# Optimization experiments

Hardware: AMD Instinct MI355X
Metric: run time of the kernel (lower is better)

## Reference

```python
import jax, jax.numpy as jnp
import numpy as np

N = 100000   # nodes
E = 800000   # edges
D = 128      # input dim
H = 128      # hidden dim
C = 2        # output classes
BN_EPS = 1e-5


def setup_inputs() -> dict:
    key = jax.random.key(0)
    ks = jax.random.split(key, 24)
    glorot = lambda k, shape: jax.random.normal(k, shape, dtype=jnp.float32) * np.sqrt(2.0 / (shape[0] + shape[1]))
    inp = {
        "x": jax.random.normal(ks[0], (N, D), dtype=jnp.float32),
        "edge_index": jax.random.randint(ks[1], (2, E), 0, N, dtype=jnp.int64),
        "W0": glorot(ks[2], (D, H)), "b0": jnp.zeros((H,), jnp.float32),
        "W1": glorot(ks[3], (H, H)), "b1": jnp.zeros((H,), jnp.float32),
        "W2": glorot(ks[4], (H, H)), "b2": jnp.zeros((H,), jnp.float32),
        "W3": glorot(ks[5], (H, C)), "b3": jnp.zeros((C,), jnp.float32),
        # BatchNorm (eval mode: running stats)
        "bn0_g": jax.random.normal(ks[6], (H,), dtype=jnp.float32) * 0.1 + 1.0,
        "bn0_b": jax.random.normal(ks[7], (H,), dtype=jnp.float32) * 0.1,
        "bn0_m": jax.random.normal(ks[8], (H,), dtype=jnp.float32) * 0.1,
        "bn0_v": jax.random.uniform(ks[9], (H,), dtype=jnp.float32) + 0.5,
        "bn1_g": jax.random.normal(ks[10], (H,), dtype=jnp.float32) * 0.1 + 1.0,
        "bn1_b": jax.random.normal(ks[11], (H,), dtype=jnp.float32) * 0.1,
        "bn1_m": jax.random.normal(ks[12], (H,), dtype=jnp.float32) * 0.1,
        "bn1_v": jax.random.uniform(ks[13], (H,), dtype=jnp.float32) + 0.5,
    }
    return inp


def _gcn_conv(h, W, b, src, dst, norm, self_norm):
    # GCNConv: D^-1/2 (A + I) D^-1/2 (h W) + b
    hw = h @ W                                             # [N, out]
    msg = hw[src] * norm[:, None]                          # [E, out] gather
    agg = jax.ops.segment_sum(msg, dst, num_segments=N)    # [N, out] scatter-add
    return agg + hw * self_norm[:, None] + b


def _bn_eval(h, g, b, m, v):
    return (h - m) * (g * jax.lax.rsqrt(v + BN_EPS)) + b


def reference(x, edge_index, W0, b0, W1, b1, W2, b2, W3, b3,
              bn0_g, bn0_b, bn0_m, bn0_v, bn1_g, bn1_b, bn1_m, bn1_v):
    src, dst = edge_index[0], edge_index[1]
    # symmetric normalization with self-loops
    deg = jax.ops.segment_sum(jnp.ones((E,), jnp.float32), dst, num_segments=N) + 1.0
    dis = jax.lax.rsqrt(deg)                 # deg >= 1, no inf
    norm = dis[src] * dis[dst]               # per-edge norm
    self_norm = dis * dis                    # self-loop norm

    # layer 0 (eval mode: dropout is identity)
    h = jax.nn.relu(_gcn_conv(x, W0, b0, src, dst, norm, self_norm))
    # layer 1: conv -> bn -> relu -> residual
    h_prev = h
    h = _gcn_conv(h, W1, b1, src, dst, norm, self_norm)
    h = jax.nn.relu(_bn_eval(h, bn0_g, bn0_b, bn0_m, bn0_v)) + h_prev
    # layer 2
    h_prev = h
    h = _gcn_conv(h, W2, b2, src, dst, norm, self_norm)
    h = jax.nn.relu(_bn_eval(h, bn1_g, bn1_b, bn1_m, bn1_v)) + h_prev
    # output layer
    h = _gcn_conv(h, W3, b3, src, dst, norm, self_norm)
    return jax.nn.log_softmax(h, axis=1)
```

## Files before the change

### kernel.cpp

```cpp
#include <hip/hip_runtime.h>
#include <hip/hip_bf16.h>
#include <type_traits>

#define NN 100000
#define NE 800000
#define HD 128
#define BN_EPS 1e-5f
#define NB_E_C 3125

typedef __bf16 bf16x8 __attribute__((ext_vector_type(8)));
typedef float  f32x4  __attribute__((ext_vector_type(4)));
typedef float  f32x2  __attribute__((ext_vector_type(2)));


__global__ __launch_bounds__(256) void count_prep_k(const int* __restrict__ ei, int* __restrict__ count,
                                                    int* __restrict__ rank,
                                                    const float* __restrict__ W0, const float* __restrict__ W1,
                                                    const float* __restrict__ W2, __bf16* __restrict__ WT,
                                                    const float* __restrict__ g0, const float* __restrict__ b0,
                                                    const float* __restrict__ m0, const float* __restrict__ v0,
                                                    const float* __restrict__ g1, const float* __restrict__ b1,
                                                    const float* __restrict__ m1, const float* __restrict__ v1,
                                                    float* __restrict__ A0, float* __restrict__ B0,
                                                    float* __restrict__ A1, float* __restrict__ B1) {
    int bid = blockIdx.x;
    int tid = threadIdx.x;
    if (bid < NB_E_C) {
        int e = bid * 256 + tid;
        if (e < NE) rank[e] = atomicAdd(&count[ei[NE + e]], 1);
    } else if (bid < NB_E_C + 3) {
        int w = bid - NB_E_C;
        const float* Ws[3] = {W0, W1, W2};
        const float* W = Ws[w];
        __bf16* T = WT + w * (HD * HD);
        #pragma unroll 4
        for (int it = 0; it < 64; ++it) {
            int idx = it * 256 + tid;
            int n = idx >> 7, k = idx & 127;
            T[idx] = (__bf16)W[k * HD + n];
        }
    } else {
        if (tid < 128) {
            float a = g0[tid] * rsqrtf(v0[tid] + BN_EPS);
            A0[tid] = a; B0[tid] = b0[tid] - m0[tid] * a;
        } else {
            int u = tid - 128;
            float a = g1[u] * rsqrtf(v1[u] + BN_EPS);
            A1[u] = a; B1[u] = b1[u] - m1[u] * a;
        }
    }
}

__global__ __launch_bounds__(256) void scan1_k(const int* __restrict__ count,
                                               int* __restrict__ rp, int* __restrict__ bsums,
                                               float* __restrict__ dis, float* __restrict__ selfn) {
    __shared__ int sm[256];
    int tid = threadIdx.x;
    int i = blockIdx.x * 256 + tid;
    int v = (i < NN) ? count[i] : 0;
    if (i < NN) {
        float deg = (float)v + 1.0f;
        float di = rsqrtf(deg);
        dis[i] = di;
        selfn[i] = di * di;
    }
    sm[tid] = v; __syncthreads();
    for (int off = 1; off < 256; off <<= 1) {
        int t = (tid >= off) ? sm[tid - off] : 0;
        __syncthreads();
        sm[tid] += t;
        __syncthreads();
    }
    if (i < NN) rp[i] = sm[tid] - v;
    if (tid == 255) bsums[blockIdx.x] = sm[tid];
}

__global__ __launch_bounds__(256) void scan23_k(int* __restrict__ rp, const int* __restrict__ bsums, int nb) {
    __shared__ int sm[256];
    int tid = threadIdx.x;
    int b = blockIdx.x;
    int partial = 0;
    for (int i = tid; i < b; i += 256) partial += bsums[i];
    sm[tid] = partial; __syncthreads();
    #pragma unroll
    for (int off = 128; off > 0; off >>= 1) {
        if (tid < off) sm[tid] += sm[tid + off];
        __syncthreads();
    }
    int prefix = sm[0];
    int i = b * 256 + tid;
    if (i < NN) rp[i] += prefix;
    if (i == 0) rp[NN] = NE;
}

__global__ __launch_bounds__(256) void scatter_k(const int* __restrict__ ei, const int* __restrict__ rp,
                                                 const int* __restrict__ rank, const float* __restrict__ dis,
                                                 uint2* __restrict__ edges) {
    int e = blockIdx.x * 256 + threadIdx.x;
    if (e >= NE) return;
    int s = ei[e], d = ei[NE + e];
    int pos = rp[d] + rank[e];
    edges[pos] = make_uint2((unsigned)s, __float_as_uint(dis[s] * dis[d]));
}


template <typename T>
__global__ __launch_bounds__(256, 5) void gemm128_k(const T* __restrict__ A, const __bf16* __restrict__ WTg,
                                                    __bf16* __restrict__ HW) {
    __shared__ __bf16 WL[128 * 128];
    const int tid = threadIdx.x;
    const int wid  = __builtin_amdgcn_readfirstlane(tid >> 6);
    const int lane = tid & 63;
    const int m = lane & 15, quad = lane >> 4;
    const int row_base = blockIdx.x * 64 + wid * 16;

    int r = row_base + m;
    if (r >= NN) r = NN - 1;
    bf16x8 afr[4];
    if constexpr (std::is_same<T, float>::value) {
        const float4* ap = (const float4*)(A + (size_t)r * HD);
        #pragma unroll
        for (int ks = 0; ks < 4; ++ks) {
            float4 x0 = ap[ks * 8 + quad * 2], x1 = ap[ks * 8 + quad * 2 + 1];
            bf16x8 a;
            a[0] = (__bf16)x0.x; a[1] = (__bf16)x0.y; a[2] = (__bf16)x0.z; a[3] = (__bf16)x0.w;
            a[4] = (__bf16)x1.x; a[5] = (__bf16)x1.y; a[6] = (__bf16)x1.z; a[7] = (__bf16)x1.w;
            afr[ks] = a;
        }
    } else {
        const bf16x8* ap = (const bf16x8*)(A + (size_t)r * HD);
        #pragma unroll
        for (int ks = 0; ks < 4; ++ks) afr[ks] = ap[ks * 4 + quad];
    }

    #pragma unroll
    for (int it = 0; it < 8; ++it) {
        int id = it * 256 + tid;
        int n = id >> 4, c = id & 15;
        int cs = c ^ ((n >> 3) & 7);
        *(uint4*)&WL[n * 128 + cs * 8] = *(const uint4*)(WTg + n * HD + c * 8);
    }
    __syncthreads();

    f32x4 acc[8];
    #pragma unroll
    for (int ct = 0; ct < 8; ++ct) acc[ct] = (f32x4){0.f, 0.f, 0.f, 0.f};

    #pragma unroll
    for (int ks = 0; ks < 4; ++ks) {
        #pragma unroll
        for (int ct = 0; ct < 8; ++ct) {
            int n = m * 8 + ct;
            int cs = (ks * 4 + quad) ^ (m & 7);
            bf16x8 bfr = *(const bf16x8*)&WL[n * 128 + cs * 8];
            acc[ct] = __builtin_amdgcn_mfma_f32_16x16x32_bf16(afr[ks], bfr, acc[ct], 0, 0, 0);
        }
    }

    #pragma unroll
    for (int rr = 0; rr < 4; ++rr) {
        int row = row_base + quad * 4 + rr;
        if (row < NN) {
            bf16x8 v;
            #pragma unroll
            for (int ct = 0; ct < 8; ++ct) v[ct] = (__bf16)acc[ct][rr];
            *(bf16x8*)(HW + (size_t)row * HD + m * 8) = v;
        }
    }
}


__device__ __forceinline__ void acc8p(f32x2* acc, uint4 rv, float wt) {
    f32x2 w2 = {wt, wt};
    f32x2 x0 = {__uint_as_float(rv.x << 16), __uint_as_float(rv.x & 0xffff0000u)};
    f32x2 x1 = {__uint_as_float(rv.y << 16), __uint_as_float(rv.y & 0xffff0000u)};
    f32x2 x2 = {__uint_as_float(rv.z << 16), __uint_as_float(rv.z & 0xffff0000u)};
    f32x2 x3 = {__uint_as_float(rv.w << 16), __uint_as_float(rv.w & 0xffff0000u)};
    acc[0] = __builtin_elementwise_fma(x0, w2, acc[0]);
    acc[1] = __builtin_elementwise_fma(x1, w2, acc[1]);
    acc[2] = __builtin_elementwise_fma(x2, w2, acc[2]);
    acc[3] = __builtin_elementwise_fma(x3, w2, acc[3]);
}

__device__ __forceinline__ void unpack8(uint4 rv, float* f) {
    f[0] = __uint_as_float(rv.x << 16);         f[1] = __uint_as_float(rv.x & 0xffff0000u);
    f[2] = __uint_as_float(rv.y << 16);         f[3] = __uint_as_float(rv.y & 0xffff0000u);
    f[4] = __uint_as_float(rv.z << 16);         f[5] = __uint_as_float(rv.z & 0xffff0000u);
    f[6] = __uint_as_float(rv.w << 16);         f[7] = __uint_as_float(rv.w & 0xffff0000u);
}

template <int MODE>
__global__ __launch_bounds__(256) void agg_k(const __bf16* __restrict__ hw, const int* __restrict__ rp,
                                             const uint2* __restrict__ edges,
                                             const float* __restrict__ selfn, const float* __restrict__ bias,
                                             const float* __restrict__ bnA, const float* __restrict__ bnB,
                                             __bf16* __restrict__ hb, const float* __restrict__ W3,
                                             float2* __restrict__ hw3) {
    const int lane = threadIdx.x & 63;
    const int wid  = threadIdx.x >> 6;
    const int grp  = lane >> 4;
    const int m    = lane & 15;
    const int n = blockIdx.x * 16 + wid * 4 + grp;
    const int c0 = m * 8;
    const int L = NE - 1;

    const int e0 = rp[n], e1 = rp[n + 1];

    const float sn = selfn[n];
    uint4 rv_self = *(const uint4*)(hw + ((size_t)n << 7) + c0);
    __bf16* hbp = hb + ((size_t)n << 7) + c0;
    uint4 rv_prev;
    float4 bs0 = *(const float4*)(bias + c0);
    float4 bs1 = *(const float4*)(bias + c0 + 4);
    float4 a0v, a1v, b0v, b1v;
    float4 w0, w1, w2, w3v;
    if (MODE != 0) {
        rv_prev = *(const uint4*)hbp;
        a0v = *(const float4*)(bnA + c0); a1v = *(const float4*)(bnA + c0 + 4);
        b0v = *(const float4*)(bnB + c0); b1v = *(const float4*)(bnB + c0 + 4);
    }
    if (MODE == 2) {
        w0  = *(const float4*)(W3 + c0 * 2);
        w1  = *(const float4*)(W3 + c0 * 2 + 4);
        w2  = *(const float4*)(W3 + c0 * 2 + 8);
        w3v = *(const float4*)(W3 + c0 * 2 + 12);
    }

    f32x2 acc2[4];
    #pragma unroll
    for (int j = 0; j < 4; ++j) acc2[j] = (f32x2){0.f, 0.f};

    int e = e0;
    int cnt = e1 - e0;
    uint2 edA = edges[min(e,     L)];
    uint2 edB = edges[min(e + 1, L)];
    uint2 edC = edges[min(e + 2, L)];
    uint2 edD = edges[min(e + 3, L)];
    while (cnt >= 4) {
        uint4 r0 = *(const uint4*)(hw + ((size_t)edA.x << 7) + c0);
        uint4 r1 = *(const uint4*)(hw + ((size_t)edB.x << 7) + c0);
        uint4 r2 = *(const uint4*)(hw + ((size_t)edC.x << 7) + c0);
        uint4 r3 = *(const uint4*)(hw + ((size_t)edD.x << 7) + c0);
        uint2 nA = edges[min(e + 4, L)];
        uint2 nB = edges[min(e + 5, L)];
        uint2 nC = edges[min(e + 6, L)];
        uint2 nD = edges[min(e + 7, L)];
        acc8p(acc2, r0, __uint_as_float(edA.y));
        acc8p(acc2, r1, __uint_as_float(edB.y));
        acc8p(acc2, r2, __uint_as_float(edC.y));
        acc8p(acc2, r3, __uint_as_float(edD.y));
        edA = nA; edB = nB; edC = nC; edD = nD;
        e += 4; cnt -= 4;
    }
    if (cnt >= 2) {
        uint4 r0 = *(const uint4*)(hw + ((size_t)edA.x << 7) + c0);
        uint4 r1 = *(const uint4*)(hw + ((size_t)edB.x << 7) + c0);
        acc8p(acc2, r0, __uint_as_float(edA.y));
        acc8p(acc2, r1, __uint_as_float(edB.y));
        edA = edC;
        cnt -= 2;
    }
    if (cnt == 1) {
        uint4 rv = *(const uint4*)(hw + ((size_t)edA.x << 7) + c0);
        acc8p(acc2, rv, __uint_as_float(edA.y));
    }
    acc8p(acc2, rv_self, sn);

    float acc[8] = {acc2[0][0], acc2[0][1], acc2[1][0], acc2[1][1],
                    acc2[2][0], acc2[2][1], acc2[3][0], acc2[3][1]};

    float z[8] = {acc[0] + bs0.x, acc[1] + bs0.y, acc[2] + bs0.z, acc[3] + bs0.w,
                  acc[4] + bs1.x, acc[5] + bs1.y, acc[6] + bs1.z, acc[7] + bs1.w};

    if (MODE == 0) {
        bf16x8 v;
        #pragma unroll
        for (int j = 0; j < 8; ++j) v[j] = (__bf16)fmaxf(z[j], 0.f);
        *(bf16x8*)hbp = v;
    } else {
        float Af[8] = {a0v.x, a0v.y, a0v.z, a0v.w, a1v.x, a1v.y, a1v.z, a1v.w};
        float Bf[8] = {b0v.x, b0v.y, b0v.z, b0v.w, b1v.x, b1v.y, b1v.z, b1v.w};
        float pr[8];
        unpack8(rv_prev, pr);
        float hn[8];
        #pragma unroll
        for (int j = 0; j < 8; ++j)
            hn[j] = fmaxf(fmaf(z[j], Af[j], Bf[j]), 0.f) + pr[j];

        if (MODE == 1) {
            bf16x8 v;
            #pragma unroll
            for (int j = 0; j < 8; ++j) v[j] = (__bf16)hn[j];
            *(bf16x8*)hbp = v;
        } else {
            float p0 = hn[0] * w0.x + hn[1] * w0.z + hn[2] * w1.x + hn[3] * w1.z
                     + hn[4] * w2.x + hn[5] * w2.z + hn[6] * w3v.x + hn[7] * w3v.z;
            float p1 = hn[0] * w0.y + hn[1] * w0.w + hn[2] * w1.y + hn[3] * w1.w
                     + hn[4] * w2.y + hn[5] * w2.w + hn[6] * w3v.y + hn[7] * w3v.w;
            #pragma unroll
            for (int o = 1; o < 16; o <<= 1) {
                p0 += __shfl_xor(p0, o);
                p1 += __shfl_xor(p1, o);
            }
            if (m == 0) hw3[n] = make_float2(p0, p1);
        }
    }
}


__global__ __launch_bounds__(256) void final_k(const float2* __restrict__ hw3, const int* __restrict__ rp,
                                               const uint2* __restrict__ edges,
                                               const float* __restrict__ selfn, const float* __restrict__ b3,
                                               float* __restrict__ out) {
    int n = blockIdx.x * 256 + threadIdx.x;
    if (n >= NN) return;
    const int L = NE - 1;
    float a0 = 0.f, a1 = 0.f;
    int e0 = rp[n], e1 = rp[n + 1];
    int cnt = e1 - e0;
    uint2 edA = edges[min(e0,     L)];
    uint2 edB = edges[min(e0 + 1, L)];
    int e = e0;
    while (cnt >= 2) {
        float2 v0 = hw3[edA.x];
        float2 v1 = hw3[edB.x];
        float w0 = __uint_as_float(edA.y), w1 = __uint_as_float(edB.y);
        edA = edges[min(e + 2, L)];
        edB = edges[min(e + 3, L)];
        a0 = fmaf(w0, v0.x, a0); a1 = fmaf(w0, v0.y, a1);
        a0 = fmaf(w1, v1.x, a0); a1 = fmaf(w1, v1.y, a1);
        e += 2; cnt -= 2;
    }
    if (cnt == 1) {
        float2 v = hw3[edA.x];
        float w = __uint_as_float(edA.y);
        a0 = fmaf(w, v.x, a0); a1 = fmaf(w, v.y, a1);
    }
    float sn = selfn[n];
    float2 hv = hw3[n];
    float z0 = a0 + sn * hv.x + b3[0];
    float z1 = a1 + sn * hv.y + b3[1];
    float mx = fmaxf(z0, z1);
    float l = mx + logf(expf(z0 - mx) + expf(z1 - mx));
    out[n * 2 + 0] = z0 - l;
    out[n * 2 + 1] = z1 - l;
}


extern "C" void kernel_launch(void* const* d_in, const int* in_sizes, int n_in,
                              void* d_out, int out_size, void* d_ws, size_t ws_size,
                              hipStream_t stream) {
    (void)in_sizes; (void)n_in; (void)out_size; (void)ws_size;

    const float* x   = (const float*)d_in[0];
    const int*   ei  = (const int*)d_in[1];
    const float* W0  = (const float*)d_in[2];
    const float* b0  = (const float*)d_in[3];
    const float* W1  = (const float*)d_in[4];
    const float* b1  = (const float*)d_in[5];
    const float* W2  = (const float*)d_in[6];
    const float* b2  = (const float*)d_in[7];
    const float* W3  = (const float*)d_in[8];
    const float* b3  = (const float*)d_in[9];
    const float* bn0g = (const float*)d_in[10];
    const float* bn0b = (const float*)d_in[11];
    const float* bn0m = (const float*)d_in[12];
    const float* bn0v = (const float*)d_in[13];
    const float* bn1g = (const float*)d_in[14];
    const float* bn1b = (const float*)d_in[15];
    const float* bn1m = (const float*)d_in[16];
    const float* bn1v = (const float*)d_in[17];
    float* out = (float*)d_out;

    char* p = (char*)d_ws;
    auto alloc = [&](size_t bytes) -> void* {
        void* r = (void*)p;
        p += (bytes + 255) & ~(size_t)255;
        return r;
    };
    __bf16*  hb    = (__bf16*)alloc((size_t)NN * HD * 2);
    __bf16*  hw    = (__bf16*)alloc((size_t)NN * HD * 2);
    float2*  hw3   = (float2*)alloc((size_t)NN * 8);
    float*   dis   = (float*)alloc((size_t)NN * 4);
    float*   selfn = (float*)alloc((size_t)NN * 4);
    int*     count = (int*)alloc((size_t)NN * 4);
    int*     rp    = (int*)alloc((size_t)(NN + 1) * 4);
    uint2*   edges = (uint2*)alloc((size_t)NE * 8);
    int*     rank  = (int*)alloc((size_t)NE * 4);
    int*     bsums = (int*)alloc((size_t)512 * 4);
    float*   bnA0  = (float*)alloc(128 * 4);
    float*   bnB0  = (float*)alloc(128 * 4);
    float*   bnA1  = (float*)alloc(128 * 4);
    float*   bnB1  = (float*)alloc(128 * 4);
    __bf16*  WT    = (__bf16*)alloc((size_t)3 * HD * HD * 2);

    const int NB_E = (NE + 255) / 256;
    const int NB_N = (NN + 255) / 256;
    const int NB_G = (NN + 63) / 64;
    const int NB_A = (NN + 15) / 16;

    hipMemsetAsync(count, 0, (size_t)NN * 4, stream);

    count_prep_k<<<NB_E + 4, 256, 0, stream>>>(ei, count, rank,
                                               W0, W1, W2, WT,
                                               bn0g, bn0b, bn0m, bn0v, bn1g, bn1b, bn1m, bn1v,
                                               bnA0, bnB0, bnA1, bnB1);
    scan1_k<<<NB_N, 256, 0, stream>>>(count, rp, bsums, dis, selfn);
    scan23_k<<<NB_N, 256, 0, stream>>>(rp, bsums, NB_N);
    scatter_k<<<NB_E, 256, 0, stream>>>(ei, rp, rank, dis, edges);

    gemm128_k<float><<<NB_G, 256, 0, stream>>>(x, WT, hw);
    agg_k<0><<<NB_A, 256, 0, stream>>>(hw, rp, edges, selfn, b0,
                                       nullptr, nullptr, hb, nullptr, nullptr);
    gemm128_k<__bf16><<<NB_G, 256, 0, stream>>>(hb, WT + HD * HD, hw);
    agg_k<1><<<NB_A, 256, 0, stream>>>(hw, rp, edges, selfn, b1,
                                       bnA0, bnB0, hb, nullptr, nullptr);
    gemm128_k<__bf16><<<NB_G, 256, 0, stream>>>(hb, WT + 2 * HD * HD, hw);
    agg_k<2><<<NB_A, 256, 0, stream>>>(hw, rp, edges, selfn, b2,
                                       bnA1, bnB1, hb, W3, hw3);
    final_k<<<NB_N, 256, 0, stream>>>(hw3, rp, edges, selfn, b3, out);
}
```

Measured before the change: 334.5 us.

## Sort edges by source block within rows and order nodes by degree

The CSR build now counts edges per (destination, source-block) pair across 16 source blocks. Each row's edges therefore come out grouped by source range, which should improve gather locality in the aggregation kernels. It also builds a degree histogram and a permutation that orders nodes by in-degree, so each aggregation wavefront handles rows of similar length and lane imbalance drops. The costs are a 16x larger count array to memset and scan, an extra indirection through perm in every agg kernel, and scattered output writes; some parameter loads are also moved later in agg_k to shorten register live ranges.

```diff
diff --git a/kernel.cpp b/kernel.cpp
--- a/kernel.cpp
+++ b/kernel.cpp
@@ -7,14 +7,17 @@
 #define HD 128
 #define BN_EPS 1e-5f
 #define NB_E_C 3125
+#define NB_N_C 391
+#define NKB 16
+#define KBW 6250
 
 typedef __bf16 bf16x8 __attribute__((ext_vector_type(8)));
 typedef float  f32x4  __attribute__((ext_vector_type(4)));
 typedef float  f32x2  __attribute__((ext_vector_type(2)));
 
 
-__global__ __launch_bounds__(256) void count_prep_k(const int* __restrict__ ei, int* __restrict__ count,
-                                                    int* __restrict__ rank,
+__global__ __launch_bounds__(256) void count_prep_k(const int* __restrict__ ei, int* __restrict__ count2,
+                                                    int* __restrict__ rank2,
                                                     const float* __restrict__ W0, const float* __restrict__ W1,
                                                     const float* __restrict__ W2, __bf16* __restrict__ WT,
                                                     const float* __restrict__ g0, const float* __restrict__ b0,
@@ -27,7 +30,11 @@
     int tid = threadIdx.x;
     if (bid < NB_E_C) {
         int e = bid * 256 + tid;
-        if (e < NE) rank[e] = atomicAdd(&count[ei[NE + e]], 1);
+        if (e < NE) {
+            int s = ei[e], d = ei[NE + e];
+            int kb = s / KBW;
+            rank2[e] = atomicAdd(&count2[d * NKB + kb], 1);
+        }
     } else if (bid < NB_E_C + 3) {
         int w = bid - NB_E_C;
         const float* Ws[3] = {W0, W1, W2};
@@ -51,19 +58,39 @@
     }
 }
 
-__global__ __launch_bounds__(256) void scan1_k(const int* __restrict__ count,
+__global__ __launch_bounds__(256) void scan1_k(int* __restrict__ count2,
                                                int* __restrict__ rp, int* __restrict__ bsums,
-                                               float* __restrict__ dis, float* __restrict__ selfn) {
+                                               float* __restrict__ dis, float* __restrict__ selfn,
+                                               int* __restrict__ hist) {
     __shared__ int sm[256];
+    __shared__ int lhist[64];
     int tid = threadIdx.x;
+    if (tid < 64) lhist[tid] = 0;
     int i = blockIdx.x * 256 + tid;
-    int v = (i < NN) ? count[i] : 0;
+    int v = 0;
     if (i < NN) {
+        int base = i * NKB;
+        int4* c4 = (int4*)&count2[base];
+        int4 a = c4[0], b = c4[1], c = c4[2], d = c4[3];
+        int run = 0;
+        int t;
+        t = a.x; a.x = run; run += t;  t = a.y; a.y = run; run += t;
+        t = a.z; a.z = run; run += t;  t = a.w; a.w = run; run += t;
+        t = b.x; b.x = run; run += t;  t = b.y; b.y = run; run += t;
+        t = b.z; b.z = run; run += t;  t = b.w; b.w = run; run += t;
+        t = c.x; c.x = run; run += t;  t = c.y; c.y = run; run += t;
+        t = c.z; c.z = run; run += t;  t = c.w; c.w = run; run += t;
+        t = d.x; d.x = run; run += t;  t = d.y; d.y = run; run += t;
+        t = d.z; d.z = run; run += t;  t = d.w; d.w = run; run += t;
+        c4[0] = a; c4[1] = b; c4[2] = c; c4[3] = d;
+        v = run;
         float deg = (float)v + 1.0f;
         float di = rsqrtf(deg);
         dis[i] = di;
         selfn[i] = di * di;
     }
+    __syncthreads();
+    if (i < NN) atomicAdd(&lhist[min(v, 63)], 1);
     sm[tid] = v; __syncthreads();
     for (int off = 1; off < 256; off <<= 1) {
         int t = (tid >= off) ? sm[tid - off] : 0;
@@ -73,6 +100,7 @@
     }
     if (i < NN) rp[i] = sm[tid] - v;
     if (tid == 255) bsums[blockIdx.x] = sm[tid];
+    if (tid < 64 && lhist[tid]) atomicAdd(&hist[tid], lhist[tid]);
 }
 
 __global__ __launch_bounds__(256) void scan23_k(int* __restrict__ rp, const int* __restrict__ bsums, int nb) {
@@ -94,13 +122,42 @@
 }
 
 __global__ __launch_bounds__(256) void scatter_k(const int* __restrict__ ei, const int* __restrict__ rp,
-                                                 const int* __restrict__ rank, const float* __restrict__ dis,
-                                                 uint2* __restrict__ edges) {
-    int e = blockIdx.x * 256 + threadIdx.x;
-    if (e >= NE) return;
-    int s = ei[e], d = ei[NE + e];
-    int pos = rp[d] + rank[e];
-    edges[pos] = make_uint2((unsigned)s, __float_as_uint(dis[s] * dis[d]));
+                                                 const int* __restrict__ count2, const int* __restrict__ rank2,
+                                                 const float* __restrict__ dis,
+                                                 uint2* __restrict__ edges,
+                                                 const int* __restrict__ hist, int* __restrict__ histcnt,
+                                                 int* __restrict__ perm) {
+    int bid = blockIdx.x;
+    int tid = threadIdx.x;
+    if (bid < NB_E_C) {
+        int e = bid * 256 + tid;
+        if (e >= NE) return;
+        int s = ei[e], d = ei[NE + e];
+        int kb = s / KBW;
+        int pos = rp[d] + count2[d * NKB + kb] + rank2[e];
+        edges[pos] = make_uint2((unsigned)s, __float_as_uint(dis[s] * dis[d]));
+    } else {
+        __shared__ int lh[64];
+        __shared__ int gb[64];
+        __shared__ int lhist[64];
+        if (tid < 64) { lh[tid] = 0; lhist[tid] = hist[tid]; }
+        __syncthreads();
+        int i = (bid - NB_E_C) * 256 + tid;
+        int bin = 0, lrank = 0;
+        if (i < NN) {
+            int deg = rp[i + 1] - rp[i];
+            bin = min(deg, 63);
+            lrank = atomicAdd(&lh[bin], 1);
+        }
+        __syncthreads();
+        if (tid < 64 && lh[tid]) gb[tid] = atomicAdd(&histcnt[tid], lh[tid]);
+        __syncthreads();
+        if (i < NN) {
+            int pf = 0;
+            for (int j = 0; j < bin; ++j) pf += lhist[j];
+            perm[pf + gb[bin] + lrank] = i;
+        }
+    }
 }
 
 
@@ -191,7 +248,7 @@
 
 template <int MODE>
 __global__ __launch_bounds__(256) void agg_k(const __bf16* __restrict__ hw, const int* __restrict__ rp,
-                                             const uint2* __restrict__ edges,
+                                             const uint2* __restrict__ edges, const int* __restrict__ perm,
                                              const float* __restrict__ selfn, const float* __restrict__ bias,
                                              const float* __restrict__ bnA, const float* __restrict__ bnB,
                                              __bf16* __restrict__ hb, const float* __restrict__ W3,
@@ -200,7 +257,8 @@
     const int wid  = threadIdx.x >> 6;
     const int grp  = lane >> 4;
     const int m    = lane & 15;
-    const int n = blockIdx.x * 16 + wid * 4 + grp;
+    const int idx = blockIdx.x * 16 + wid * 4 + grp;
+    const int n = perm[idx];
     const int c0 = m * 8;
     const int L = NE - 1;
 
@@ -210,21 +268,7 @@
     uint4 rv_self = *(const uint4*)(hw + ((size_t)n << 7) + c0);
     __bf16* hbp = hb + ((size_t)n << 7) + c0;
     uint4 rv_prev;
-    float4 bs0 = *(const float4*)(bias + c0);
-    float4 bs1 = *(const float4*)(bias + c0 + 4);
-    float4 a0v, a1v, b0v, b1v;
-    float4 w0, w1, w2, w3v;
-    if (MODE != 0) {
-        rv_prev = *(const uint4*)hbp;
-        a0v = *(const float4*)(bnA + c0); a1v = *(const float4*)(bnA + c0 + 4);
-        b0v = *(const float4*)(bnB + c0); b1v = *(const float4*)(bnB + c0 + 4);
-    }
-    if (MODE == 2) {
-        w0  = *(const float4*)(W3 + c0 * 2);
-        w1  = *(const float4*)(W3 + c0 * 2 + 4);
-        w2  = *(const float4*)(W3 + c0 * 2 + 8);
-        w3v = *(const float4*)(W3 + c0 * 2 + 12);
-    }
+    if (MODE != 0) rv_prev = *(const uint4*)hbp;
 
     f32x2 acc2[4];
     #pragma unroll
@@ -269,6 +313,8 @@
     float acc[8] = {acc2[0][0], acc2[0][1], acc2[1][0], acc2[1][1],
                     acc2[2][0], acc2[2][1], acc2[3][0], acc2[3][1]};
 
+    float4 bs0 = *(const float4*)(bias + c0);
+    float4 bs1 = *(const float4*)(bias + c0 + 4);
     float z[8] = {acc[0] + bs0.x, acc[1] + bs0.y, acc[2] + bs0.z, acc[3] + bs0.w,
                   acc[4] + bs1.x, acc[5] + bs1.y, acc[6] + bs1.z, acc[7] + bs1.w};
 
@@ -278,6 +324,8 @@
         for (int j = 0; j < 8; ++j) v[j] = (__bf16)fmaxf(z[j], 0.f);
         *(bf16x8*)hbp = v;
     } else {
+        float4 a0v = *(const float4*)(bnA + c0), a1v = *(const float4*)(bnA + c0 + 4);
+        float4 b0v = *(const float4*)(bnB + c0), b1v = *(const float4*)(bnB + c0 + 4);
         float Af[8] = {a0v.x, a0v.y, a0v.z, a0v.w, a1v.x, a1v.y, a1v.z, a1v.w};
         float Bf[8] = {b0v.x, b0v.y, b0v.z, b0v.w, b1v.x, b1v.y, b1v.z, b1v.w};
         float pr[8];
@@ -293,6 +341,10 @@
             for (int j = 0; j < 8; ++j) v[j] = (__bf16)hn[j];
             *(bf16x8*)hbp = v;
         } else {
+            float4 w0 = *(const float4*)(W3 + c0 * 2);
+            float4 w1 = *(const float4*)(W3 + c0 * 2 + 4);
+            float4 w2 = *(const float4*)(W3 + c0 * 2 + 8);
+            float4 w3v = *(const float4*)(W3 + c0 * 2 + 12);
             float p0 = hn[0] * w0.x + hn[1] * w0.z + hn[2] * w1.x + hn[3] * w1.z
                      + hn[4] * w2.x + hn[5] * w2.z + hn[6] * w3v.x + hn[7] * w3v.z;
             float p1 = hn[0] * w0.y + hn[1] * w0.w + hn[2] * w1.y + hn[3] * w1.w
@@ -383,10 +435,13 @@
     float2*  hw3   = (float2*)alloc((size_t)NN * 8);
     float*   dis   = (float*)alloc((size_t)NN * 4);
     float*   selfn = (float*)alloc((size_t)NN * 4);
-    int*     count = (int*)alloc((size_t)NN * 4);
+    int*     count2 = (int*)alloc((size_t)NN * NKB * 4 + 512);
+    int*     hist   = count2 + (size_t)NN * NKB;
+    int*     histcnt = hist + 64;
     int*     rp    = (int*)alloc((size_t)(NN + 1) * 4);
     uint2*   edges = (uint2*)alloc((size_t)NE * 8);
-    int*     rank  = (int*)alloc((size_t)NE * 4);
+    int*     rank2 = (int*)alloc((size_t)NE * 4);
+    int*     perm  = (int*)alloc((size_t)NN * 4);
     int*     bsums = (int*)alloc((size_t)512 * 4);
     float*   bnA0  = (float*)alloc(128 * 4);
     float*   bnB0  = (float*)alloc(128 * 4);
@@ -394,29 +449,29 @@
     float*   bnB1  = (float*)alloc(128 * 4);
     __bf16*  WT    = (__bf16*)alloc((size_t)3 * HD * HD * 2);
 
-    const int NB_E = (NE + 255) / 256;
-    const int NB_N = (NN + 255) / 256;
+    const int NB_N = NB_N_C;
     const int NB_G = (NN + 63) / 64;
     const int NB_A = (NN + 15) / 16;
 
-    hipMemsetAsync(count, 0, (size_t)NN * 4, stream);
-
-    count_prep_k<<<NB_E + 4, 256, 0, stream>>>(ei, count, rank,
-                                               W0, W1, W2, WT,
-                                               bn0g, bn0b, bn0m, bn0v, bn1g, bn1b, bn1m, bn1v,
-                                               bnA0, bnB0, bnA1, bnB1);
-    scan1_k<<<NB_N, 256, 0, stream>>>(count, rp, bsums, dis, selfn);
+    hipMemsetAsync(count2, 0, (size_t)NN * NKB * 4 + 512, stream);
+
+    count_prep_k<<<NB_E_C + 4, 256, 0, stream>>>(ei, count2, rank2,
+                                                 W0, W1, W2, WT,
+                                                 bn0g, bn0b, bn0m, bn0v, bn1g, bn1b, bn1m, bn1v,
+                                                 bnA0, bnB0, bnA1, bnB1);
+    scan1_k<<<NB_N, 256, 0, stream>>>(count2, rp, bsums, dis, selfn, hist);
     scan23_k<<<NB_N, 256, 0, stream>>>(rp, bsums, NB_N);
-    scatter_k<<<NB_E, 256, 0, stream>>>(ei, rp, rank, dis, edges);
+    scatter_k<<<NB_E_C + NB_N, 256, 0, stream>>>(ei, rp, count2, rank2, dis, edges,
+                                                 hist, histcnt, perm);
 
     gemm128_k<float><<<NB_G, 256, 0, stream>>>(x, WT, hw);
-    agg_k<0><<<NB_A, 256, 0, stream>>>(hw, rp, edges, selfn, b0,
+    agg_k<0><<<NB_A, 256, 0, stream>>>(hw, rp, edges, perm, selfn, b0,
                                        nullptr, nullptr, hb, nullptr, nullptr);
     gemm128_k<__bf16><<<NB_G, 256, 0, stream>>>(hb, WT + HD * HD, hw);
-    agg_k<1><<<NB_A, 256, 0, stream>>>(hw, rp, edges, selfn, b1,
+    agg_k<1><<<NB_A, 256, 0, stream>>>(hw, rp, edges, perm, selfn, b1,
                                        bnA0, bnB0, hb, nullptr, nullptr);
     gemm128_k<__bf16><<<NB_G, 256, 0, stream>>>(hb, WT + 2 * HD * HD, hw);
-    agg_k<2><<<NB_A, 256, 0, stream>>>(hw, rp, edges, selfn, b2,
+    agg_k<2><<<NB_A, 256, 0, stream>>>(hw, rp, edges, perm, selfn, b2,
                                        bnA1, bnB1, hb, W3, hw3);
     final_k<<<NB_N, 256, 0, stream>>>(hw3, rp, edges, selfn, b3, out);
 }
```

Measured after the change: 353.3 us. 5.6% more time.

## Fuse layer 1-2 GEMMs into aggregation by aggregating before the transform

Applied to the files above, without the earlier changes.

Layers 1 and 2 now aggregate the input features first (A·h) and apply the weight matrix afterwards inside the same kernel, using MFMA on a 16-row tile staged in LDS. This removes two standalone GEMM launches and the round trip of the hw intermediate through global memory. The residual input is reused from the self row already loaded, and the layer-2 kernel reduces to the 2-class projection directly. The cost is loading the 32KB weight tile into LDS per 16-node block, extra syncs, a second ping-pong buffer, and an extra bf16 rounding of the aggregated features before the matmul.

```diff
diff --git a/kernel.cpp b/kernel.cpp
--- a/kernel.cpp
+++ b/kernel.cpp
@@ -9,6 +9,7 @@
 #define NB_E_C 3125
 
 typedef __bf16 bf16x8 __attribute__((ext_vector_type(8)));
+typedef __bf16 bf16x2 __attribute__((ext_vector_type(2)));
 typedef float  f32x4  __attribute__((ext_vector_type(4)));
 typedef float  f32x2  __attribute__((ext_vector_type(2)));
 
@@ -137,7 +138,7 @@
     for (int it = 0; it < 8; ++it) {
         int id = it * 256 + tid;
         int n = id >> 4, c = id & 15;
-        int cs = c ^ ((n >> 3) & 7);
+        int cs = c ^ (n >> 3);
         *(uint4*)&WL[n * 128 + cs * 8] = *(const uint4*)(WTg + n * HD + c * 8);
     }
     __syncthreads();
@@ -151,7 +152,7 @@
         #pragma unroll
         for (int ct = 0; ct < 8; ++ct) {
             int n = m * 8 + ct;
-            int cs = (ks * 4 + quad) ^ (m & 7);
+            int cs = (ks * 4 + quad) ^ m;
             bf16x8 bfr = *(const bf16x8*)&WL[n * 128 + cs * 8];
             acc[ct] = __builtin_amdgcn_mfma_f32_16x16x32_bf16(afr[ks], bfr, acc[ct], 0, 0, 0);
         }
@@ -182,20 +183,11 @@
     acc[3] = __builtin_elementwise_fma(x3, w2, acc[3]);
 }
 
-__device__ __forceinline__ void unpack8(uint4 rv, float* f) {
-    f[0] = __uint_as_float(rv.x << 16);         f[1] = __uint_as_float(rv.x & 0xffff0000u);
-    f[2] = __uint_as_float(rv.y << 16);         f[3] = __uint_as_float(rv.y & 0xffff0000u);
-    f[4] = __uint_as_float(rv.z << 16);         f[5] = __uint_as_float(rv.z & 0xffff0000u);
-    f[6] = __uint_as_float(rv.w << 16);         f[7] = __uint_as_float(rv.w & 0xffff0000u);
-}
-
-template <int MODE>
-__global__ __launch_bounds__(256) void agg_k(const __bf16* __restrict__ hw, const int* __restrict__ rp,
-                                             const uint2* __restrict__ edges,
-                                             const float* __restrict__ selfn, const float* __restrict__ bias,
-                                             const float* __restrict__ bnA, const float* __restrict__ bnB,
-                                             __bf16* __restrict__ hb, const float* __restrict__ W3,
-                                             float2* __restrict__ hw3) {
+
+__global__ __launch_bounds__(256) void agg0_k(const __bf16* __restrict__ hw, const int* __restrict__ rp,
+                                              const uint2* __restrict__ edges,
+                                              const float* __restrict__ selfn, const float* __restrict__ bias,
+                                              __bf16* __restrict__ hb) {
     const int lane = threadIdx.x & 63;
     const int wid  = threadIdx.x >> 6;
     const int grp  = lane >> 4;
@@ -205,26 +197,8 @@
     const int L = NE - 1;
 
     const int e0 = rp[n], e1 = rp[n + 1];
-
     const float sn = selfn[n];
     uint4 rv_self = *(const uint4*)(hw + ((size_t)n << 7) + c0);
-    __bf16* hbp = hb + ((size_t)n << 7) + c0;
-    uint4 rv_prev;
-    float4 bs0 = *(const float4*)(bias + c0);
-    float4 bs1 = *(const float4*)(bias + c0 + 4);
-    float4 a0v, a1v, b0v, b1v;
-    float4 w0, w1, w2, w3v;
-    if (MODE != 0) {
-        rv_prev = *(const uint4*)hbp;
-        a0v = *(const float4*)(bnA + c0); a1v = *(const float4*)(bnA + c0 + 4);
-        b0v = *(const float4*)(bnB + c0); b1v = *(const float4*)(bnB + c0 + 4);
-    }
-    if (MODE == 2) {
-        w0  = *(const float4*)(W3 + c0 * 2);
-        w1  = *(const float4*)(W3 + c0 * 2 + 4);
-        w2  = *(const float4*)(W3 + c0 * 2 + 8);
-        w3v = *(const float4*)(W3 + c0 * 2 + 12);
-    }
 
     f32x2 acc2[4];
     #pragma unroll
@@ -266,43 +240,176 @@
     }
     acc8p(acc2, rv_self, sn);
 
-    float acc[8] = {acc2[0][0], acc2[0][1], acc2[1][0], acc2[1][1],
-                    acc2[2][0], acc2[2][1], acc2[3][0], acc2[3][1]};
-
-    float z[8] = {acc[0] + bs0.x, acc[1] + bs0.y, acc[2] + bs0.z, acc[3] + bs0.w,
-                  acc[4] + bs1.x, acc[5] + bs1.y, acc[6] + bs1.z, acc[7] + bs1.w};
-
-    if (MODE == 0) {
-        bf16x8 v;
+    float a8[8] = {acc2[0][0], acc2[0][1], acc2[1][0], acc2[1][1],
+                   acc2[2][0], acc2[2][1], acc2[3][0], acc2[3][1]};
+    float4 bs0 = *(const float4*)(bias + c0);
+    float4 bs1 = *(const float4*)(bias + c0 + 4);
+    float bf[8] = {bs0.x, bs0.y, bs0.z, bs0.w, bs1.x, bs1.y, bs1.z, bs1.w};
+    bf16x8 v;
+    #pragma unroll
+    for (int j = 0; j < 8; ++j) v[j] = (__bf16)fmaxf(a8[j] + bf[j], 0.f);
+    *(bf16x8*)(hb + ((size_t)n << 7) + c0) = v;
+}
+
+
+template <int MODE>
+__global__ __launch_bounds__(256, 4) void aggw_k(const __bf16* __restrict__ hbI, const __bf16* __restrict__ WTg,
+                                                 const int* __restrict__ rp, const uint2* __restrict__ edges,
+                                                 const float* __restrict__ selfn, const float* __restrict__ bias,
+                                                 const float* __restrict__ bnA, const float* __restrict__ bnB,
+                                                 __bf16* __restrict__ hbO, const float* __restrict__ W3,
+                                                 float2* __restrict__ hw3) {
+    __shared__ __bf16 WLs[128 * 128];
+    __shared__ __bf16 SL[16 * 128];
+    __shared__ __bf16 SelfL[16 * 128];
+    const int tid = threadIdx.x;
+    const int wid  = __builtin_amdgcn_readfirstlane(tid >> 6);
+    const int lane = tid & 63;
+    const int quad = lane >> 4;
+    const int m    = lane & 15;
+    const int nn = wid * 4 + quad;
+    const int n = blockIdx.x * 16 + nn;
+    const int c0 = m * 8;
+    const int L = NE - 1;
+
+    #pragma unroll
+    for (int it = 0; it < 8; ++it) {
+        int id = it * 256 + tid;
+        int r = id >> 4, c = id & 15;
+        int cs = c ^ (r >> 3);
+        *(uint4*)&WLs[r * 128 + cs * 8] = *(const uint4*)(WTg + r * HD + c * 8);
+    }
+
+    const int e0 = rp[n], e1 = rp[n + 1];
+    const float sn = selfn[n];
+    uint4 rv_self = *(const uint4*)(hbI + ((size_t)n << 7) + c0);
+
+    f32x2 acc2[4];
+    #pragma unroll
+    for (int j = 0; j < 4; ++j) acc2[j] = (f32x2){0.f, 0.f};
+
+    int e = e0;
+    int cnt = e1 - e0;
+    uint2 edA = edges[min(e,     L)];
+    uint2 edB = edges[min(e + 1, L)];
+    uint2 edC = edges[min(e + 2, L)];
+    uint2 edD = edges[min(e + 3, L)];
+    while (cnt >= 4) {
+        uint4 r0 = *(const uint4*)(hbI + ((size_t)edA.x << 7) + c0);
+        uint4 r1 = *(const uint4*)(hbI + ((size_t)edB.x << 7) + c0);
+        uint4 r2 = *(const uint4*)(hbI + ((size_t)edC.x << 7) + c0);
+        uint4 r3 = *(const uint4*)(hbI + ((size_t)edD.x << 7) + c0);
+        uint2 nA = edges[min(e + 4, L)];
+        uint2 nB = edges[min(e + 5, L)];
+        uint2 nC = edges[min(e + 6, L)];
+        uint2 nD = edges[min(e + 7, L)];
+        acc8p(acc2, r0, __uint_as_float(edA.y));
+        acc8p(acc2, r1, __uint_as_float(edB.y));
+        acc8p(acc2, r2, __uint_as_float(edC.y));
+        acc8p(acc2, r3, __uint_as_float(edD.y));
+        edA = nA; edB = nB; edC = nC; edD = nD;
+        e += 4; cnt -= 4;
+    }
+    if (cnt >= 2) {
+        uint4 r0 = *(const uint4*)(hbI + ((size_t)edA.x << 7) + c0);
+        uint4 r1 = *(const uint4*)(hbI + ((size_t)edB.x << 7) + c0);
+        acc8p(acc2, r0, __uint_as_float(edA.y));
+        acc8p(acc2, r1, __uint_as_float(edB.y));
+        edA = edC;
+        cnt -= 2;
+    }
+    if (cnt == 1) {
+        uint4 rv = *(const uint4*)(hbI + ((size_t)edA.x << 7) + c0);
+        acc8p(acc2, rv, __uint_as_float(edA.y));
+    }
+    acc8p(acc2, rv_self, sn);
+
+    {
+        float a8[8] = {acc2[0][0], acc2[0][1], acc2[1][0], acc2[1][1],
+                       acc2[2][0], acc2[2][1], acc2[3][0], acc2[3][1]};
+        bf16x8 sv;
         #pragma unroll
-        for (int j = 0; j < 8; ++j) v[j] = (__bf16)fmaxf(z[j], 0.f);
-        *(bf16x8*)hbp = v;
+        for (int j = 0; j < 8; ++j) sv[j] = (__bf16)a8[j];
+        int pc = m ^ nn;
+        *(bf16x8*)&SL[nn * 128 + pc * 8] = sv;
+        *(uint4*)&SelfL[nn * 128 + pc * 8] = rv_self;
+    }
+    __syncthreads();
+
+    bf16x8 afr[4];
+    #pragma unroll
+    for (int ks = 0; ks < 4; ++ks) {
+        int pcR = (ks * 4 + quad) ^ m;
+        afr[ks] = *(const bf16x8*)&SL[m * 128 + pcR * 8];
+    }
+    f32x4 acc[2];
+    acc[0] = (f32x4){0.f, 0.f, 0.f, 0.f};
+    acc[1] = (f32x4){0.f, 0.f, 0.f, 0.f};
+    #pragma unroll
+    for (int ks = 0; ks < 4; ++ks) {
+        int pcR = (ks * 4 + quad) ^ m;
+        #pragma unroll
+        for (int t = 0; t < 2; ++t) {
+            int ct = wid * 2 + t;
+            int nW = m * 8 + ct;
+            bf16x8 bfr = *(const bf16x8*)&WLs[nW * 128 + pcR * 8];
+            acc[t] = __builtin_amdgcn_mfma_f32_16x16x32_bf16(afr[ks], bfr, acc[t], 0, 0, 0);
+        }
+    }
+
+    const int ch0 = m * 8 + wid * 2;
+    float2 bias2 = *(const float2*)(bias + ch0);
+    float2 A2 = *(const float2*)(bnA + ch0);
+    float2 B2 = *(const float2*)(bnB + ch0);
+    float4 w3r;
+    if (MODE == 2) w3r = *(const float4*)(W3 + ch0 * 2);
+    float p0a[4], p1a[4];
+    #pragma unroll
+    for (int rr = 0; rr < 4; ++rr) {
+        int nd = quad * 4 + rr;
+        char* sp = (char*)SelfL + nd * 256 + ((m ^ nd) * 16) + wid * 4;
+        unsigned sv = *(const unsigned*)sp;
+        float s0 = __uint_as_float(sv << 16);
+        float s1 = __uint_as_float(sv & 0xffff0000u);
+        float z0 = acc[0][rr] + bias2.x;
+        float z1 = acc[1][rr] + bias2.y;
+        float h0 = fmaxf(fmaf(z0, A2.x, B2.x), 0.f) + s0;
+        float h1 = fmaxf(fmaf(z1, A2.y, B2.y), 0.f) + s1;
+        if (MODE == 1) {
+            bf16x2 pr = {(__bf16)h0, (__bf16)h1};
+            *(bf16x2*)sp = pr;
+        } else {
+            p0a[rr] = h0 * w3r.x + h1 * w3r.z;
+            p1a[rr] = h0 * w3r.y + h1 * w3r.w;
+        }
+    }
+
+    if (MODE == 1) {
+        __syncthreads();
+        uint4 outv = *(const uint4*)&SelfL[nn * 128 + (m ^ nn) * 8];
+        *(uint4*)(hbO + ((size_t)n << 7) + c0) = outv;
     } else {
-        float Af[8] = {a0v.x, a0v.y, a0v.z, a0v.w, a1v.x, a1v.y, a1v.z, a1v.w};
-        float Bf[8] = {b0v.x, b0v.y, b0v.z, b0v.w, b1v.x, b1v.y, b1v.z, b1v.w};
-        float pr[8];
-        unpack8(rv_prev, pr);
-        float hn[8];
         #pragma unroll
-        for (int j = 0; j < 8; ++j)
-            hn[j] = fmaxf(fmaf(z[j], Af[j], Bf[j]), 0.f) + pr[j];
-
-        if (MODE == 1) {
-            bf16x8 v;
-            #pragma unroll
-            for (int j = 0; j < 8; ++j) v[j] = (__bf16)hn[j];
-            *(bf16x8*)hbp = v;
-        } else {
-            float p0 = hn[0] * w0.x + hn[1] * w0.z + hn[2] * w1.x + hn[3] * w1.z
-                     + hn[4] * w2.x + hn[5] * w2.z + hn[6] * w3v.x + hn[7] * w3v.z;
-            float p1 = hn[0] * w0.y + hn[1] * w0.w + hn[2] * w1.y + hn[3] * w1.w
-                     + hn[4] * w2.y + hn[5] * w2.w + hn[6] * w3v.y + hn[7] * w3v.w;
+        for (int rr = 0; rr < 4; ++rr) {
             #pragma unroll
             for (int o = 1; o < 16; o <<= 1) {
-                p0 += __shfl_xor(p0, o);
-                p1 += __shfl_xor(p1, o);
+                p0a[rr] += __shfl_xor(p0a[rr], o);
+                p1a[rr] += __shfl_xor(p1a[rr], o);
             }
-            if (m == 0) hw3[n] = make_float2(p0, p1);
+        }
+        __syncthreads();
+        float2* PL = (float2*)SL;
+        if (m == 0) {
+            #pragma unroll
+            for (int rr = 0; rr < 4; ++rr)
+                PL[(quad * 4 + rr) * 4 + wid] = make_float2(p0a[rr], p1a[rr]);
+        }
+        __syncthreads();
+        if (tid < 16) {
+            float2 a = PL[tid * 4 + 0], b = PL[tid * 4 + 1];
+            float2 c = PL[tid * 4 + 2], d = PL[tid * 4 + 3];
+            hw3[blockIdx.x * 16 + tid] = make_float2(a.x + b.x + c.x + d.x,
+                                                     a.y + b.y + c.y + d.y);
         }
     }
 }
@@ -379,6 +486,7 @@
         return r;
     };
     __bf16*  hb    = (__bf16*)alloc((size_t)NN * HD * 2);
+    __bf16*  hb2   = (__bf16*)alloc((size_t)NN * HD * 2);
     __bf16*  hw    = (__bf16*)alloc((size_t)NN * HD * 2);
     float2*  hw3   = (float2*)alloc((size_t)NN * 8);
     float*   dis   = (float*)alloc((size_t)NN * 4);
@@ -394,29 +502,25 @@
     float*   bnB1  = (float*)alloc(128 * 4);
     __bf16*  WT    = (__bf16*)alloc((size_t)3 * HD * HD * 2);
 
-    const int NB_E = (NE + 255) / 256;
     const int NB_N = (NN + 255) / 256;
     const int NB_G = (NN + 63) / 64;
     const int NB_A = (NN + 15) / 16;
 
     hipMemsetAsync(count, 0, (size_t)NN * 4, stream);
 
-    count_prep_k<<<NB_E + 4, 256, 0, stream>>>(ei, count, rank,
-                                               W0, W1, W2, WT,
-                                               bn0g, bn0b, bn0m, bn0v, bn1g, bn1b, bn1m, bn1v,
-                                               bnA0, bnB0, bnA1, bnB1);
+    count_prep_k<<<NB_E_C + 4, 256, 0, stream>>>(ei, count, rank,
+                                                 W0, W1, W2, WT,
+                                                 bn0g, bn0b, bn0m, bn0v, bn1g, bn1b, bn1m, bn1v,
+                                                 bnA0, bnB0, bnA1, bnB1);
     scan1_k<<<NB_N, 256, 0, stream>>>(count, rp, bsums, dis, selfn);
     scan23_k<<<NB_N, 256, 0, stream>>>(rp, bsums, NB_N);
-    scatter_k<<<NB_E, 256, 0, stream>>>(ei, rp, rank, dis, edges);
+    scatter_k<<<NB_E_C, 256, 0, stream>>>(ei, rp, rank, dis, edges);
 
     gemm128_k<float><<<NB_G, 256, 0, stream>>>(x, WT, hw);
-    agg_k<0><<<NB_A, 256, 0, stream>>>(hw, rp, edges, selfn, b0,
-                                       nullptr, nullptr, hb, nullptr, nullptr);
-    gemm128_k<__bf16><<<NB_G, 256, 0, stream>>>(hb, WT + HD * HD, hw);
-    agg_k<1><<<NB_A, 256, 0, stream>>>(hw, rp, edges, selfn, b1,
-                                       bnA0, bnB0, hb, nullptr, nullptr);
-    gemm128_k<__bf16><<<NB_G, 256, 0, stream>>>(hb, WT + 2 * HD * HD, hw);
-    agg_k<2><<<NB_A, 256, 0, stream>>>(hw, rp, edges, selfn, b2,
-                                       bnA1, bnB1, hb, W3, hw3);
+    agg0_k<<<NB_A, 256, 0, stream>>>(hw, rp, edges, selfn, b0, hb);
+    aggw_k<1><<<NB_A, 256, 0, stream>>>(hb, WT + HD * HD, rp, edges, selfn, b1,
+                                        bnA0, bnB0, hb2, nullptr, nullptr);
+    aggw_k<2><<<NB_A, 256, 0, stream>>>(hb2, WT + 2 * HD * HD, rp, edges, selfn, b2,
+                                        bnA1, bnB1, nullptr, W3, hw3);
     final_k<<<NB_N, 256, 0, stream>>>(hw3, rp, edges, selfn, b3, out);
 }
```

Result: faster. 322.4 us (-3.6%).
